# Kernel tuning notes

Measured on AMD Instinct MI355X. Metric: run time of the kernel, lower is better.

The kernel has to match this reference:

```python
import jax, jax.numpy as jnp
import numpy as np

B, N, M, L, H = 32, 4096, 256, 128, 4
GAMMA = 2.0


def setup_inputs() -> dict:
    key = jax.random.key(0)
    kx, km, kv, ku, kw = jax.random.split(key, 5)
    x = jax.random.normal(kx, (B, N, M), dtype=jnp.float32)
    masks = (jax.random.uniform(km, (B, N)) > 0.3).astype(jnp.float32)
    # VarianceScaling(scale=0.1, fan_in, uniform) ~ small init; exact dist doesn't affect math
    V = jax.random.normal(kv, (H, M, L), dtype=jnp.float32) * 0.02
    U = jax.random.normal(ku, (H, M, L), dtype=jnp.float32) * 0.02
    w = jax.random.normal(kw, (H, L, 1), dtype=jnp.float32) * 0.05
    return {"x": x, "masks": masks, "V": V, "U": U, "w": w}


def reference(x, masks, V, U, w):
    # x: [B,N,M], masks: [B,N], V/U: [H,M,L], w: [H,L,1]
    m = masks[:, None, :, None]  # [B,1,N,1] broadcast over heads
    gated = jnp.tanh(jnp.einsum('bnm,hml->bhnl', x, V)) * jax.nn.sigmoid(
        jnp.einsum('bnm,hml->bhnl', x, U))          # [B,H,N,L]
    logits = jnp.einsum('bhnl,hl->bhn', gated, w[..., 0])[..., None]  # [B,H,N,1]
    a = m * logits                                   # masked logits (as in original)
    a = m * jnp.exp(a)                               # masked exp
    a = a / jnp.sum(a, axis=2, keepdims=True)        # softmax over instances
    ag = a ** GAMMA
    a = ag / jnp.sum(ag, axis=2, keepdims=True)      # gamma-power renorm
    emb = jnp.einsum('bhnk,bnm->bhm', a, x)          # weighted sum; k is the trailing 1
    emb = emb.reshape(B, H * M)                      # concat heads along axis=1
    att = jnp.transpose(a, (1, 0, 2, 3))             # [H,B,N,1] (per-head attention list)
    return (att, emb)
```

## Files before the change

kernel.cpp:

```cpp
#include <hip/hip_runtime.h>
#include <hip/hip_bf16.h>
#include <stdint.h>

#define B_ 32
#define N_ 4096
#define M_ 256
#define L_ 128
#define H_ 4
#define BN_ (B_ * N_)

typedef __bf16 bf16x8 __attribute__((ext_vector_type(8)));
typedef float  f32x4  __attribute__((ext_vector_type(4)));

__device__ __forceinline__ unsigned short f2bf(float f) {
    unsigned int u = __float_as_uint(f);
    u += 0x7fffu + ((u >> 16) & 1u);
    return (unsigned short)(u >> 16);
}
__device__ __forceinline__ unsigned int pack2(float lo, float hi) {
    return (unsigned int)f2bf(lo) | ((unsigned int)f2bf(hi) << 16);
}

__device__ __forceinline__ void gload16(const void* g, void* l) {
    __builtin_amdgcn_global_load_lds(
        (const __attribute__((address_space(1))) unsigned int*)g,
        (__attribute__((address_space(3))) unsigned int*)l, 16, 0, 0);
}


__global__ void prep_x(const float* __restrict__ x, unsigned short* __restrict__ xb) {
    const int blk  = blockIdx.x;
    const int tile = blk >> 2, ks = blk & 3;
    const int i    = threadIdx.x;
    const int kk   = (i & 7) * 8;
    const int tl   = kk >> 5;
    const int kl   = kk & 31;
    char* dst = (char*)xb + ((size_t)tile * 8 + ks * 2 + tl) * 8192;
#pragma unroll
    for (int rep = 0; rep < 4; ++rep) {
        int row = rep * 32 + (i >> 3);
        const float* gx = x + (size_t)(tile * 128 + row) * M_ + ks * 64 + kk;
        float4 a = *(const float4*)gx;
        float4 b = *(const float4*)(gx + 4);
        uint4 o;
        o.x = pack2(a.x, a.y); o.y = pack2(a.z, a.w);
        o.z = pack2(b.x, b.y); o.w = pack2(b.z, b.w);
        int byte = (row * 64 + kl * 2) ^ ((row & 6) << 3);
        *(uint4*)(dst + byte) = o;
    }
}

__global__ void prep_vu_img(const float* __restrict__ V, const float* __restrict__ U,
                            unsigned short* __restrict__ vu) {
    __shared__ float slab[64][129];
    const int b   = blockIdx.x;
    const int mat = b & 1, ks = (b >> 1) & 3, h = b >> 3;
    const float* src = (mat ? U : V) + ((size_t)h * M_ + ks * 64) * L_;
    const int tid = threadIdx.x;
#pragma unroll
    for (int rep = 0; rep < 32; ++rep) {
        int idx = rep * 256 + tid;
        slab[idx >> 7][idx & 127] = src[(size_t)(idx >> 7) * L_ + (idx & 127)];
    }
    __syncthreads();
#pragma unroll
    for (int rep = 0; rep < 4; ++rep) {
        int cidx = rep * 256 + tid;
        int l  = cidx >> 3;
        int kk = (cidx & 7) * 8;
        uint4 o;
        o.x = pack2(slab[kk + 0][l], slab[kk + 1][l]);
        o.y = pack2(slab[kk + 2][l], slab[kk + 3][l]);
        o.z = pack2(slab[kk + 4][l], slab[kk + 5][l]);
        o.w = pack2(slab[kk + 6][l], slab[kk + 7][l]);
        int tl = kk >> 5, kl = kk & 31;
        char* dst = (char*)vu + (((size_t)(h * 8 + ks * 2 + tl)) * 2 + mat) * 8192;
        int byte = (l * 64 + kl * 2) ^ ((l & 6) << 3);
        *(uint4*)(dst + byte) = o;
    }
}

__global__ __launch_bounds__(256, 3)
void gemm_fast2(const unsigned short* __restrict__ xb,
                const unsigned short* __restrict__ vu,
                const float* __restrict__ w,
                float* __restrict__ logits) {
    __shared__ __align__(16) unsigned short xs[2][4096];
    __shared__ __align__(16) unsigned short vs[2][4096];
    __shared__ __align__(16) unsigned short us[2][4096];
    __shared__ float wl[L_];

    const int orig    = blockIdx.x;
    const int logical = (orig & 7) * 512 + (orig >> 3);
    const int tile    = logical >> 2;
    const int h       = logical & 3;

    const int tid  = threadIdx.x;
    const int lane = tid & 63;
    const int wv   = tid >> 6;
    const int g    = lane >> 4;
    const int c    = lane & 15;

    if (tid < L_) wl[tid] = w[h * L_ + tid];

    f32x4 accV[2][8], accU[2][8];
#pragma unroll
    for (int rf = 0; rf < 2; ++rf)
#pragma unroll
        for (int cf = 0; cf < 8; ++cf) {
            accV[rf][cf] = (f32x4){0.f, 0.f, 0.f, 0.f};
            accU[rf][cf] = (f32x4){0.f, 0.f, 0.f, 0.f};
        }

    const char* xim = (const char*)xb + (size_t)tile * 65536;
    const char* vim = (const char*)vu + (size_t)h * 131072;
    const int soff = wv * 2048;

    {
        const char* vsrc = vim;
        const char* usrc = vim + 8192;
        gload16(xim  + soff +        lane * 16, (char*)xs[0] + soff);
        gload16(xim  + soff + 1024 + lane * 16, (char*)xs[0] + soff + 1024);
        gload16(vsrc + soff +        lane * 16, (char*)vs[0] + soff);
        gload16(vsrc + soff + 1024 + lane * 16, (char*)vs[0] + soff + 1024);
        gload16(usrc + soff +        lane * 16, (char*)us[0] + soff);
        gload16(usrc + soff + 1024 + lane * 16, (char*)us[0] + soff + 1024);
    }
    __syncthreads();

    for (int t = 0; t < 8; ++t) {
        const int buf = t & 1;
        if (t < 7) {
            const char* xsrc = xim + (t + 1) * 8192;
            const char* vsrc = vim + (t + 1) * 16384;
            const char* usrc = vsrc + 8192;
            gload16(xsrc + soff +        lane * 16, (char*)xs[buf ^ 1] + soff);
            gload16(xsrc + soff + 1024 + lane * 16, (char*)xs[buf ^ 1] + soff + 1024);
            gload16(vsrc + soff +        lane * 16, (char*)vs[buf ^ 1] + soff);
            gload16(vsrc + soff + 1024 + lane * 16, (char*)vs[buf ^ 1] + soff + 1024);
            gload16(usrc + soff +        lane * 16, (char*)us[buf ^ 1] + soff);
            gload16(usrc + soff + 1024 + lane * 16, (char*)us[buf ^ 1] + soff + 1024);
        }
        bf16x8 a0, a1;
        {
            int r = wv * 32 + c;
            int byte = (r * 64 + g * 16) ^ ((r & 6) << 3);
            a0 = *(const bf16x8*)((const char*)xs[buf] + byte);
            r += 16;
            byte = (r * 64 + g * 16) ^ ((r & 6) << 3);
            a1 = *(const bf16x8*)((const char*)xs[buf] + byte);
        }
#pragma unroll
        for (int cf = 0; cf < 8; ++cf) {
            int l = cf * 16 + c;
            int byte = (l * 64 + g * 16) ^ ((l & 6) << 3);
            bf16x8 bv = *(const bf16x8*)((const char*)vs[buf] + byte);
            bf16x8 bu = *(const bf16x8*)((const char*)us[buf] + byte);
            accV[0][cf] = __builtin_amdgcn_mfma_f32_16x16x32_bf16(a0, bv, accV[0][cf], 0, 0, 0);
            accV[1][cf] = __builtin_amdgcn_mfma_f32_16x16x32_bf16(a1, bv, accV[1][cf], 0, 0, 0);
            accU[0][cf] = __builtin_amdgcn_mfma_f32_16x16x32_bf16(a0, bu, accU[0][cf], 0, 0, 0);
            accU[1][cf] = __builtin_amdgcn_mfma_f32_16x16x32_bf16(a1, bu, accU[1][cf], 0, 0, 0);
        }
        __syncthreads();
    }

#pragma unroll
    for (int rf = 0; rf < 2; ++rf) {
        float plog[4] = {0.f, 0.f, 0.f, 0.f};
#pragma unroll
        for (int cf = 0; cf < 8; ++cf) {
            float wvv = wl[cf * 16 + c];
#pragma unroll
            for (int i = 0; i < 4; ++i) {
                float vv = accV[rf][cf][i];
                float uu = accU[rf][cf][i];
                vv = fminf(fmaxf(vv, -20.f), 20.f);
                float A = __expf(2.f * vv);
                float E = __expf(fminf(-uu, 30.f));
                float gg = __fdividef(A - 1.f, (A + 1.f) * (1.f + E));
                plog[i] += gg * wvv;
            }
        }
#pragma unroll
        for (int i = 0; i < 4; ++i) {
            float v = plog[i];
            v += __shfl_xor(v, 1);
            v += __shfl_xor(v, 2);
            v += __shfl_xor(v, 4);
            v += __shfl_xor(v, 8);
            if (c == 0) {
                int rowflat = tile * 128 + wv * 32 + rf * 16 + g * 4 + i;
                int b = rowflat >> 12;
                int n = rowflat & (N_ - 1);
                logits[((size_t)b * H_ + h) * N_ + n] = v;
            }
        }
    }
}

__global__ void prep_vu_slow(const float* __restrict__ V, const float* __restrict__ U,
                             unsigned short* __restrict__ Vt, unsigned short* __restrict__ Ut) {
    int idx = blockIdx.x * 256 + threadIdx.x;
    int m = idx & (M_ - 1);
    int l = (idx >> 8) & (L_ - 1);
    int h = idx >> 15;
    Vt[idx] = f2bf(V[((size_t)h * M_ + m) * L_ + l]);
    Ut[idx] = f2bf(U[((size_t)h * M_ + m) * L_ + l]);
}

#define BM 128
#define BK 64

__global__ __launch_bounds__(256, 2)
void gemm_logits(const float* __restrict__ x,
                 const unsigned short* __restrict__ Vt,
                 const unsigned short* __restrict__ Ut,
                 const float* __restrict__ w,
                 float* __restrict__ logits) {
    __shared__ __align__(16) unsigned short xs[BM * BK];
    __shared__ __align__(16) unsigned short vs[L_ * BK];
    __shared__ __align__(16) unsigned short us[L_ * BK];
    __shared__ float wl[L_];

    const int h    = blockIdx.x >> 10;
    const int tile = blockIdx.x & 1023;
    const int row0 = tile * BM;
    const int tid  = threadIdx.x;
    const int lane = tid & 63;
    const int wave = tid >> 6;

    if (tid < L_) wl[tid] = w[h * L_ + tid];

    f32x4 accV[2][8], accU[2][8];
#pragma unroll
    for (int rf = 0; rf < 2; ++rf)
#pragma unroll
        for (int cf = 0; cf < 8; ++cf) {
            accV[rf][cf] = (f32x4){0.f, 0.f, 0.f, 0.f};
            accU[rf][cf] = (f32x4){0.f, 0.f, 0.f, 0.f};
        }

    const unsigned short* Vh = Vt + (size_t)h * L_ * M_;
    const unsigned short* Uh = Ut + (size_t)h * L_ * M_;
    const int g = lane >> 4;
    const int c = lane & 15;

    for (int ks = 0; ks < 4; ++ks) {
        const int k0 = ks * BK;
        __syncthreads();
#pragma unroll
        for (int p = 0; p < 4; ++p) {
            int row = p * 32 + (tid >> 3);
            int kk  = (tid & 7) * 8;
            const float* gx = x + (size_t)(row0 + row) * M_ + k0 + kk;
            float4 a = *(const float4*)gx;
            float4 b = *(const float4*)(gx + 4);
            uint4 o;
            o.x = pack2(a.x, a.y); o.y = pack2(a.z, a.w);
            o.z = pack2(b.x, b.y); o.w = pack2(b.z, b.w);
            int byte = (row * BK + kk) * 2;
            byte ^= (row & 7) << 4;
            *(uint4*)((char*)xs + byte) = o;
        }
#pragma unroll
        for (int p = 0; p < 4; ++p) {
            int l  = p * 32 + (tid >> 3);
            int kk = (tid & 7) * 8;
            uint4 v = *(const uint4*)(Vh + (size_t)l * M_ + k0 + kk);
            uint4 u = *(const uint4*)(Uh + (size_t)l * M_ + k0 + kk);
            int byte = (l * BK + kk) * 2;
            byte ^= (l & 7) << 4;
            *(uint4*)((char*)vs + byte) = v;
            *(uint4*)((char*)us + byte) = u;
        }
        __syncthreads();
#pragma unroll
        for (int ksub = 0; ksub < 2; ++ksub) {
            bf16x8 afr[2];
#pragma unroll
            for (int rf = 0; rf < 2; ++rf) {
                int row = wave * 32 + rf * 16 + c;
                int byte = (row * BK + ksub * 32 + g * 8) * 2;
                byte ^= (row & 7) << 4;
                afr[rf] = *(const bf16x8*)((const char*)xs + byte);
            }
#pragma unroll
            for (int cf = 0; cf < 8; ++cf) {
                int l = cf * 16 + c;
                int byte = (l * BK + ksub * 32 + g * 8) * 2;
                byte ^= (l & 7) << 4;
                bf16x8 bv = *(const bf16x8*)((const char*)vs + byte);
                bf16x8 bu = *(const bf16x8*)((const char*)us + byte);
#pragma unroll
                for (int rf = 0; rf < 2; ++rf) {
                    accV[rf][cf] = __builtin_amdgcn_mfma_f32_16x16x32_bf16(afr[rf], bv, accV[rf][cf], 0, 0, 0);
                    accU[rf][cf] = __builtin_amdgcn_mfma_f32_16x16x32_bf16(afr[rf], bu, accU[rf][cf], 0, 0, 0);
                }
            }
        }
    }
#pragma unroll
    for (int rf = 0; rf < 2; ++rf) {
        float plog[4] = {0.f, 0.f, 0.f, 0.f};
#pragma unroll
        for (int cf = 0; cf < 8; ++cf) {
            float wvv = wl[cf * 16 + c];
#pragma unroll
            for (int i = 0; i < 4; ++i) {
                float vv = accV[rf][cf][i];
                float uu = accU[rf][cf][i];
                vv = fminf(fmaxf(vv, -20.f), 20.f);
                float e2v = __expf(2.f * vv);
                float t = __fdividef(e2v - 1.f, e2v + 1.f);
                float s = __fdividef(1.f, 1.f + __expf(-uu));
                plog[i] += t * s * wvv;
            }
        }
#pragma unroll
        for (int i = 0; i < 4; ++i) {
            float v = plog[i];
            v += __shfl_xor(v, 1);
            v += __shfl_xor(v, 2);
            v += __shfl_xor(v, 4);
            v += __shfl_xor(v, 8);
            if (c == 0) {
                int rowflat = row0 + wave * 32 + rf * 16 + g * 4 + i;
                int b = rowflat >> 12;
                int n = rowflat & (N_ - 1);
                logits[((size_t)b * H_ + h) * N_ + n] = v;
            }
        }
    }
}

__global__ __launch_bounds__(256)
void softmax_att(const float* __restrict__ logits, const float* __restrict__ masks,
                 float* __restrict__ att) {
    const int bh = blockIdx.x;
    const int b = bh >> 2, h = bh & 3;
    __shared__ float e2s[N_];
    __shared__ float red[4];
    const int tid = threadIdx.x;

    float sum = 0.f;
#pragma unroll
    for (int i = 0; i < N_ / 256; ++i) {
        int n = i * 256 + tid;
        float lg = logits[((size_t)b * H_ + h) * N_ + n];
        float mv = masks[(size_t)b * N_ + n];
        float e = mv * __expf(mv * lg);
        float e2 = e * e;
        e2s[n] = e2;
        sum += e2;
    }
#pragma unroll
    for (int off = 32; off >= 1; off >>= 1) sum += __shfl_xor(sum, off);
    if ((tid & 63) == 0) red[tid >> 6] = sum;
    __syncthreads();
    float S = red[0] + red[1] + red[2] + red[3];
    float inv = 1.f / S;
#pragma unroll
    for (int i = 0; i < N_ / 256; ++i) {
        int n = i * 256 + tid;
        att[((size_t)h * B_ + b) * N_ + n] = e2s[n] * inv;
    }
}

#define NCH 32
#define CHUNK (N_ / NCH)

__global__ __launch_bounds__(256)
void emb_partial(const float* __restrict__ x, const float* __restrict__ att,
                 float* __restrict__ part) {
    const int bc = blockIdx.x;
    const int b = bc >> 5, ch = bc & 31;
    __shared__ float as[H_][CHUNK];
    const int tid = threadIdx.x;

    for (int i = tid; i < H_ * CHUNK; i += 256) {
        int hh = i >> 7;
        int j  = i & (CHUNK - 1);
        as[hh][j] = att[((size_t)hh * B_ + b) * N_ + ch * CHUNK + j];
    }
    __syncthreads();

    float a0 = 0.f, a1 = 0.f, a2 = 0.f, a3 = 0.f;
    const float* xp = x + ((size_t)b * N_ + ch * CHUNK) * M_ + tid;
#pragma unroll 4
    for (int j = 0; j < CHUNK; ++j) {
        float xv = xp[(size_t)j * M_];
        a0 += as[0][j] * xv;
        a1 += as[1][j] * xv;
        a2 += as[2][j] * xv;
        a3 += as[3][j] * xv;
    }
    float* pp = part + (size_t)bc * H_ * M_ + tid;
    pp[0 * M_] = a0; pp[1 * M_] = a1; pp[2 * M_] = a2; pp[3 * M_] = a3;
}

__global__ __launch_bounds__(256)
void emb_reduce(const float* __restrict__ part, float* __restrict__ emb) {
    int idx = blockIdx.x * 256 + threadIdx.x;
    int b = idx >> 10;
    int r = idx & 1023;
    float s = 0.f;
#pragma unroll
    for (int ci = 0; ci < NCH; ++ci)
        s += part[((size_t)(b * NCH + ci)) * (H_ * M_) + r];
    emb[idx] = s;
}

extern "C" void kernel_launch(void* const* d_in, const int* in_sizes, int n_in,
                              void* d_out, int out_size, void* d_ws, size_t ws_size,
                              hipStream_t stream) {
    const float* x     = (const float*)d_in[0];
    const float* masks = (const float*)d_in[1];
    const float* V     = (const float*)d_in[2];
    const float* U     = (const float*)d_in[3];
    const float* w     = (const float*)d_in[4];

    float* att = (float*)d_out;
    float* emb = att + (size_t)H_ * B_ * N_;

    char* ws = (char*)d_ws;
    const size_t XB_BYTES  = (size_t)1024 * 8 * 8192;
    const size_t VU_BYTES  = (size_t)64 * 8192;
    const size_t LG_BYTES  = (size_t)B_ * H_ * N_ * 4;
    const size_t PT_BYTES  = (size_t)B_ * NCH * H_ * M_ * 4;
    const size_t NEED_FAST = XB_BYTES + VU_BYTES + LG_BYTES + PT_BYTES;

    float* logits;
    float* partp;

    if (ws_size >= NEED_FAST) {
        unsigned short* xb = (unsigned short*)ws;
        unsigned short* vu = (unsigned short*)(ws + XB_BYTES);
        logits = (float*)(ws + XB_BYTES + VU_BYTES);
        partp  = (float*)(ws + XB_BYTES + VU_BYTES + LG_BYTES);

        prep_x     <<<4096, 256, 0, stream>>>(x, xb);
        prep_vu_img<<<32,   256, 0, stream>>>(V, U, vu);
        gemm_fast2 <<<4096, 256, 0, stream>>>(xb, vu, w, logits);
    } else {
        unsigned short* Vt = (unsigned short*)ws;
        unsigned short* Ut = (unsigned short*)(ws + 262144);
        logits = (float*)(ws + 524288);
        partp  = (float*)(ws + 524288 + LG_BYTES);

        prep_vu_slow<<<512, 256, 0, stream>>>(V, U, Vt, Ut);
        gemm_logits <<<4096, 256, 0, stream>>>(x, Vt, Ut, w, logits);
    }

    softmax_att<<<B_ * H_,              256, 0, stream>>>(logits, masks, att);
    emb_partial<<<B_ * NCH,             256, 0, stream>>>(x, att, partp);
    emb_reduce <<<(B_ * H_ * M_) / 256, 256, 0, stream>>>(partp, emb);
}
```

Measured before the change: 185.2 us.

## Triple-buffer GEMM LDS stages with explicit vmcnt waits and single barrier

Replaces double-buffered LDS staging in the logits GEMM with a three-stage ring. Loads run two k-steps ahead, and each iteration uses a partial s_waitcnt vmcnt plus one barrier instead of the trailing __syncthreads. LDS offsets are precomputed, the loop is fully unrolled, and w is read from global memory instead of staged in LDS. The goal is to hide global-to-LDS latency better. In exchange, LDS use goes up and launch bounds drop from 3 to 2 blocks per CU, which lowers occupancy.

```diff
diff --git a/kernel.cpp b/kernel.cpp
--- a/kernel.cpp
+++ b/kernel.cpp
@@ -80,15 +80,14 @@
     }
 }
 
-__global__ __launch_bounds__(256, 3)
-void gemm_fast2(const unsigned short* __restrict__ xb,
+__global__ __launch_bounds__(256, 2)
+void gemm_fast3(const unsigned short* __restrict__ xb,
                 const unsigned short* __restrict__ vu,
                 const float* __restrict__ w,
                 float* __restrict__ logits) {
-    __shared__ __align__(16) unsigned short xs[2][4096];
-    __shared__ __align__(16) unsigned short vs[2][4096];
-    __shared__ __align__(16) unsigned short us[2][4096];
-    __shared__ float wl[L_];
+    __shared__ __align__(16) unsigned short xs[3][4096];
+    __shared__ __align__(16) unsigned short vs[3][4096];
+    __shared__ __align__(16) unsigned short us[3][4096];
 
     const int orig    = blockIdx.x;
     const int logical = (orig & 7) * 512 + (orig >> 3);
@@ -101,8 +100,6 @@
     const int g    = lane >> 4;
     const int c    = lane & 15;
 
-    if (tid < L_) wl[tid] = w[h * L_ + tid];
-
     f32x4 accV[2][8], accU[2][8];
 #pragma unroll
     for (int rf = 0; rf < 2; ++rf)
@@ -112,64 +109,72 @@
             accU[rf][cf] = (f32x4){0.f, 0.f, 0.f, 0.f};
         }
 
-    const char* xim = (const char*)xb + (size_t)tile * 65536;
-    const char* vim = (const char*)vu + (size_t)h * 131072;
     const int soff = wv * 2048;
 
-    {
-        const char* vsrc = vim;
-        const char* usrc = vim + 8192;
-        gload16(xim  + soff +        lane * 16, (char*)xs[0] + soff);
-        gload16(xim  + soff + 1024 + lane * 16, (char*)xs[0] + soff + 1024);
-        gload16(vsrc + soff +        lane * 16, (char*)vs[0] + soff);
-        gload16(vsrc + soff + 1024 + lane * 16, (char*)vs[0] + soff + 1024);
-        gload16(usrc + soff +        lane * 16, (char*)us[0] + soff);
-        gload16(usrc + soff + 1024 + lane * 16, (char*)us[0] + soff + 1024);
-    }
-    __syncthreads();
-
+    const char* gxs = (const char*)xb + (size_t)tile * 65536 + soff + lane * 16;
+    const char* gvs = (const char*)vu + (size_t)h * 131072 + soff + lane * 16;
+    const char* gus = gvs + 8192;
+
+    int ar = wv * 32 + c;
+    const int aoff0 = (ar * 64 + g * 16) ^ ((ar & 6) << 3);
+    const int aoff1 = ((ar + 16) * 64 + g * 16) ^ (((ar + 16) & 6) << 3);
+    int boff[8];
+#pragma unroll
+    for (int cf = 0; cf < 8; ++cf) {
+        int l = cf * 16 + c;
+        boff[cf] = (l * 64 + g * 16) ^ ((l & 6) << 3);
+    }
+
+#define STAGE(t, bufi) do {                                          \
+        const char* _gx = gxs + (t) * 8192;                          \
+        const char* _gv = gvs + (t) * 16384;                         \
+        const char* _gu = gus + (t) * 16384;                         \
+        gload16(_gx,        (char*)xs[bufi] + soff);                 \
+        gload16(_gx + 1024, (char*)xs[bufi] + soff + 1024);          \
+        gload16(_gv,        (char*)vs[bufi] + soff);                 \
+        gload16(_gv + 1024, (char*)vs[bufi] + soff + 1024);          \
+        gload16(_gu,        (char*)us[bufi] + soff);                 \
+        gload16(_gu + 1024, (char*)us[bufi] + soff + 1024);          \
+    } while (0)
+
+    STAGE(0, 0);
+    STAGE(1, 1);
+
+#pragma unroll
     for (int t = 0; t < 8; ++t) {
-        const int buf = t & 1;
-        if (t < 7) {
-            const char* xsrc = xim + (t + 1) * 8192;
-            const char* vsrc = vim + (t + 1) * 16384;
-            const char* usrc = vsrc + 8192;
-            gload16(xsrc + soff +        lane * 16, (char*)xs[buf ^ 1] + soff);
-            gload16(xsrc + soff + 1024 + lane * 16, (char*)xs[buf ^ 1] + soff + 1024);
-            gload16(vsrc + soff +        lane * 16, (char*)vs[buf ^ 1] + soff);
-            gload16(vsrc + soff + 1024 + lane * 16, (char*)vs[buf ^ 1] + soff + 1024);
-            gload16(usrc + soff +        lane * 16, (char*)us[buf ^ 1] + soff);
-            gload16(usrc + soff + 1024 + lane * 16, (char*)us[buf ^ 1] + soff + 1024);
-        }
-        bf16x8 a0, a1;
-        {
-            int r = wv * 32 + c;
-            int byte = (r * 64 + g * 16) ^ ((r & 6) << 3);
-            a0 = *(const bf16x8*)((const char*)xs[buf] + byte);
-            r += 16;
-            byte = (r * 64 + g * 16) ^ ((r & 6) << 3);
-            a1 = *(const bf16x8*)((const char*)xs[buf] + byte);
-        }
+        if (t < 7) asm volatile("s_waitcnt vmcnt(6)" ::: "memory");
+        else       asm volatile("s_waitcnt vmcnt(0)" ::: "memory");
+        __builtin_amdgcn_s_barrier();
+        __builtin_amdgcn_sched_barrier(0);
+
+        if (t < 6) STAGE(t + 2, (t + 2) % 3);
+
+        const int buf = t % 3;
+        const char* xbuf = (const char*)xs[buf];
+        const char* vbuf = (const char*)vs[buf];
+        const char* ubuf = (const char*)us[buf];
+
+        bf16x8 a0 = *(const bf16x8*)(xbuf + aoff0);
+        bf16x8 a1 = *(const bf16x8*)(xbuf + aoff1);
 #pragma unroll
         for (int cf = 0; cf < 8; ++cf) {
-            int l = cf * 16 + c;
-            int byte = (l * 64 + g * 16) ^ ((l & 6) << 3);
-            bf16x8 bv = *(const bf16x8*)((const char*)vs[buf] + byte);
-            bf16x8 bu = *(const bf16x8*)((const char*)us[buf] + byte);
+            bf16x8 bv = *(const bf16x8*)(vbuf + boff[cf]);
+            bf16x8 bu = *(const bf16x8*)(ubuf + boff[cf]);
             accV[0][cf] = __builtin_amdgcn_mfma_f32_16x16x32_bf16(a0, bv, accV[0][cf], 0, 0, 0);
             accV[1][cf] = __builtin_amdgcn_mfma_f32_16x16x32_bf16(a1, bv, accV[1][cf], 0, 0, 0);
             accU[0][cf] = __builtin_amdgcn_mfma_f32_16x16x32_bf16(a0, bu, accU[0][cf], 0, 0, 0);
             accU[1][cf] = __builtin_amdgcn_mfma_f32_16x16x32_bf16(a1, bu, accU[1][cf], 0, 0, 0);
         }
-        __syncthreads();
-    }
-
+    }
+#undef STAGE
+
+    const float* wrow = w + h * L_;
 #pragma unroll
     for (int rf = 0; rf < 2; ++rf) {
         float plog[4] = {0.f, 0.f, 0.f, 0.f};
 #pragma unroll
         for (int cf = 0; cf < 8; ++cf) {
-            float wvv = wl[cf * 16 + c];
+            float wvv = wrow[cf * 16 + c];
 #pragma unroll
             for (int i = 0; i < 4; ++i) {
                 float vv = accV[rf][cf][i];
@@ -440,7 +445,7 @@
 
         prep_x     <<<4096, 256, 0, stream>>>(x, xb);
         prep_vu_img<<<32,   256, 0, stream>>>(V, U, vu);
-        gemm_fast2 <<<4096, 256, 0, stream>>>(xb, vu, w, logits);
+        gemm_fast3 <<<4096, 256, 0, stream>>>(xb, vu, w, logits);
     } else {
         unsigned short* Vt = (unsigned short*)ws;
         unsigned short* Ut = (unsigned short*)(ws + 262144);
```

New measurement: 176.7 us. 1.05x faster.
